# Performance work log

Measured on AMD Instinct MI355X. Metric: run time of the kernel, lower is better.

Reference implementation:

```python
import jax, jax.numpy as jnp
import numpy as np

B = 2048   # batch
C = 64     # EEG channels (num_eegch)
T = 125    # time samples -> pool5 -> 25 -> (p=5, 5)
H = 8      # num_heads
L = 6      # num_layers
D = 16     # num_projected_features
QK = 8     # qkv_len
P = 5      # tokens before cls
EPS = 1e-5


def setup_inputs() -> dict:
    key = jax.random.key(0)
    ks = iter(jax.random.split(key, 64))

    def nrm(shape, s=0.05):
        return jax.random.normal(next(ks), shape, jnp.float32) * s

    return {
        "x": jax.random.normal(next(ks), (B, 1, C, T), jnp.float32),
        "conv_t_w": nrm((8, 1, 1, 63)),
        "conv_t_b": nrm((8,)),
        "bn1_g": 1.0 + nrm((8,)),
        "bn1_b": nrm((8,)),
        "bn1_m": nrm((8,)),
        "bn1_v": 1.0 + 0.1 * jax.random.uniform(next(ks), (8,), jnp.float32),
        "conv_s_w": nrm((16, 1, C, 1)),
        "conv_s_b": nrm((16,)),
        "bn2_g": 1.0 + nrm((16,)),
        "bn2_b": nrm((16,)),
        "bn2_m": nrm((16,)),
        "bn2_v": 1.0 + 0.1 * jax.random.uniform(next(ks), (16,), jnp.float32),
        "proj_w": nrm((D, 16 * 5)),
        "proj_b": nrm((D,)),
        "cls_token": nrm((1, 1, D), 1.0),
        "pe": nrm((1, P + 1, D), 1.0),
        "qkv_w": nrm((L, 3 * H * QK, D)),
        "qkv_b": nrm((L, 3 * H * QK)),
        "out_w": nrm((L, D, H * QK)),
        "out_b": nrm((L, D)),
        "ln1_g": jnp.ones((L, D), jnp.float32),
        "ln1_b": jnp.zeros((L, D), jnp.float32),
        "ln2_g": jnp.ones((L, D), jnp.float32),
        "ln2_b": jnp.zeros((L, D), jnp.float32),
        "mlp_w1": nrm((L, 2 * D, D)),
        "mlp_b1": nrm((L, 2 * D)),
        "mlp_w2": nrm((L, D, 2 * D)),
        "mlp_b2": nrm((L, D)),
        "head_ln_g": jnp.ones((D,), jnp.float32),
        "head_ln_b": jnp.zeros((D,), jnp.float32),
        "head_w": nrm((2, D)),
        "head_b": nrm((2,)),
    }


def _bn(z, g, b, m, v):
    s = (g * jax.lax.rsqrt(v + EPS))[None, :, None, None]
    return (z - m[None, :, None, None]) * s + b[None, :, None, None]


def _ln(z, g, b):
    m = z.mean(-1, keepdims=True)
    var = jnp.mean((z - m) ** 2, -1, keepdims=True)
    return (z - m) * jax.lax.rsqrt(var + EPS) * g + b


def _forward(x, conv_t_w, conv_t_b, bn1_g, bn1_b, bn1_m, bn1_v,
             conv_s_w, conv_s_b, bn2_g, bn2_b, bn2_m, bn2_v,
             proj_w, proj_b, cls_token, pe,
             qkv_w, qkv_b, out_w, out_b, ln1_g, ln1_b, ln2_g, ln2_b,
             mlp_w1, mlp_b1, mlp_w2, mlp_b2,
             head_ln_g, head_ln_b, head_w, head_b):
    b = x.shape[0]
    dn = ('NCHW', 'OIHW', 'NCHW')
    # temporal conv, 'same' padding on width (kernel 63 -> pad 31/31)
    y = jax.lax.conv_general_dilated(x, conv_t_w, (1, 1), [(0, 0), (31, 31)], dimension_numbers=dn)
    y = _bn(y + conv_t_b[None, :, None, None], bn1_g, bn1_b, bn1_m, bn1_v)
    # grouped spatial conv collapses the EEG-channel axis
    y = jax.lax.conv_general_dilated(y, conv_s_w, (1, 1), 'VALID', dimension_numbers=dn, feature_group_count=8)
    y = _bn(y + conv_s_b[None, :, None, None], bn2_g, bn2_b, bn2_m, bn2_v)
    y = jax.nn.elu(y)                              # (b,16,1,125)
    y = y.reshape(b, 16, 1, T // 5, 5).mean(-1)    # avg_pool2d (1,5) -> (b,16,1,25)
    # dropout: identity at inference
    y = y.reshape(b, 16, 1, P, 5)
    y = jnp.swapaxes(y, 3, 4)
    tok = jnp.swapaxes(y.reshape(b, 16 * 5, P), 1, 2)   # (b,5,80)
    tok = tok @ proj_w.T + proj_b                       # (b,5,16)
    z = jnp.concatenate([jnp.broadcast_to(cls_token, (b, 1, D)), tok], axis=1) + pe  # (b,6,16)
    scale = QK ** -0.5
    for i in range(L):
        h1 = _ln(z, ln1_g[i], ln1_b[i])
        qkv = h1 @ qkv_w[i].T + qkv_b[i]                # (b,6,3*H*QK)
        q, k, v = jnp.split(qkv, 3, axis=-1)
        q = q.reshape(b, P + 1, H, QK).transpose(0, 2, 1, 3)
        k = k.reshape(b, P + 1, H, QK).transpose(0, 2, 1, 3)
        v = v.reshape(b, P + 1, H, QK).transpose(0, 2, 1, 3)
        att = jax.nn.softmax(jnp.einsum('bhsd,bhtd->bhst', q, k) * scale, axis=-1)
        o = jnp.einsum('bhst,bhtd->bhsd', att, v).transpose(0, 2, 1, 3).reshape(b, P + 1, H * QK)
        z = o @ out_w[i].T + out_b[i] + z
        h2 = _ln(z, ln2_g[i], ln2_b[i])
        m = jax.nn.gelu(h2 @ mlp_w1[i].T + mlp_b1[i], approximate=False) @ mlp_w2[i].T + mlp_b2[i]
        z = m + z
    cls = _ln(z[:, 0, :], head_ln_g, head_ln_b)
    return jax.nn.softmax(cls @ head_w.T + head_b, axis=-1)


def reference(x, conv_t_w, conv_t_b, bn1_g, bn1_b, bn1_m, bn1_v,
              conv_s_w, conv_s_b, bn2_g, bn2_b, bn2_m, bn2_v,
              proj_w, proj_b, cls_token, pe,
              qkv_w, qkv_b, out_w, out_b, ln1_g, ln1_b, ln2_g, ln2_b,
              mlp_w1, mlp_b1, mlp_w2, mlp_b2,
              head_ln_g, head_ln_b, head_w, head_b):
    return _forward(x, conv_t_w, conv_t_b, bn1_g, bn1_b, bn1_m, bn1_v,
                    conv_s_w, conv_s_b, bn2_g, bn2_b, bn2_m, bn2_v,
                    proj_w, proj_b, cls_token, pe,
                    qkv_w, qkv_b, out_w, out_b, ln1_g, ln1_b, ln2_g, ln2_b,
                    mlp_w1, mlp_b1, mlp_w2, mlp_b2,
                    head_ln_g, head_ln_b, head_w, head_b)
```

## Files before the change

### kernel.cpp

```cpp
#include <hip/hip_runtime.h>

#define WAVE_SYNC() do { asm volatile("" ::: "memory"); \
                         __builtin_amdgcn_wave_barrier(); \
                         asm volatile("" ::: "memory"); } while (0)

__device__ __forceinline__ float ln_norm16(float z, float g, float bb) {
    float s = z, q = z * z;
    #pragma unroll
    for (int off = 8; off >= 1; off >>= 1) {
        s += __shfl_xor(s, off, 16);
        q += __shfl_xor(q, off, 16);
    }
    float mean = s * 0.0625f;
    float var  = q * 0.0625f - mean * mean;
    return (z - mean) * rsqrtf(var + 1e-5f) * g + bb;
}

__device__ __forceinline__ float gelu_exact(float a) {
    float xa = fabsf(a) * 0.70710678118654752f;
    float tt = 1.f / (1.f + 0.3275911f * xa);
    float poly = tt * (0.254829592f + tt * (-0.284496736f + tt * (1.421413741f
               + tt * (-1.453152027f + tt * 1.061405429f))));
    float erfv = 1.f - poly * __expf(-xa * xa);
    erfv = a >= 0.f ? erfv : -erfv;
    return 0.5f * a * (1.f + erfv);
}

__device__ __forceinline__ float dot16(const float* h, float4 w0, float4 w1,
                                       float4 w2, float4 w3) {
    return h[0]*w0.x + h[1]*w0.y + h[2]*w0.z + h[3]*w0.w
         + h[4]*w1.x + h[5]*w1.y + h[6]*w1.z + h[7]*w1.w
         + h[8]*w2.x + h[9]*w2.y + h[10]*w2.z + h[11]*w2.w
         + h[12]*w3.x + h[13]*w3.y + h[14]*w3.z + h[15]*w3.w;
}

#define FXSP  0
#define FPOOL 3136
#define F_TOT 3584

extern "C" __global__ __launch_bounds__(128, 2)
void eegnet_frontend(
    const float* __restrict__ x,
    const float* __restrict__ conv_t_w, const float* __restrict__ conv_t_b,
    const float* __restrict__ bn1_g, const float* __restrict__ bn1_b,
    const float* __restrict__ bn1_m, const float* __restrict__ bn1_v,
    const float* __restrict__ conv_s_w, const float* __restrict__ conv_s_b,
    const float* __restrict__ bn2_g, const float* __restrict__ bn2_b,
    const float* __restrict__ bn2_m, const float* __restrict__ bn2_v,
    const float* __restrict__ proj_w, const float* __restrict__ proj_b,
    float* __restrict__ tokws)
{
    __shared__ __align__(16) float sm[F_TOT];
    const int b   = blockIdx.x;
    const int tid = threadIdx.x;

    for (int i = tid; i < 16 * 71; i += 128) {
        int row = i / 71, k = i - row * 71;
        int off = (k < 32) ? k : (k + 125);
        sm[FXSP + row * 196 + off] = 0.f;
    }

    {
        const float* xb = x + (size_t)b * 8000;
        const int t = min(tid, 124);
        float a0[16];
        #pragma unroll
        for (int o = 0; o < 16; ++o) a0[o] = 0.f;
        #pragma unroll 8
        for (int c = 0; c < 64; ++c) {
            float xv = xb[c * 125 + t];
            #pragma unroll
            for (int o = 0; o < 16; ++o)
                a0[o] += conv_s_w[o * 64 + c] * xv;
        }
        if (tid < 125) {
            #pragma unroll
            for (int o = 0; o < 16; ++o)
                sm[FXSP + o * 196 + 32 + t] = a0[o];
        }
    }

    const int oo = tid & 15, qg = tid >> 4, gg = oo >> 1;
    float sa, cc;
    {
        float s1 = bn1_g[gg] * rsqrtf(bn1_v[gg] + 1e-5f);
        float b1 = (conv_t_b[gg] - bn1_m[gg]) * s1 + bn1_b[gg];
        float s2 = bn2_g[oo] * rsqrtf(bn2_v[oo] + 1e-5f);
        float ssum = 0.f;
        const float4* csw = reinterpret_cast<const float4*>(conv_s_w + oo * 64);
        #pragma unroll
        for (int i = 0; i < 16; ++i) {
            float4 v = csw[i];
            ssum += v.x + v.y + v.z + v.w;
        }
        sa = s1 * s2;
        cc = (b1 * ssum + conv_s_b[oo] - bn2_m[oo]) * s2 + bn2_b[oo];
    }
    float wt[63];
    #pragma unroll
    for (int k = 0; k < 63; ++k) wt[k] = conv_t_w[gg * 63 + k];

    __syncthreads();

    #pragma unroll 1
    for (int jj = 0; jj < 4; ++jj) {
        int j = qg + 8 * jj;
        if (j < 25) {
            int base = FXSP + oo * 196 + 5 * j + 1;
            float acc5[5] = {0.f, 0.f, 0.f, 0.f, 0.f};
            #pragma unroll
            for (int m = 0; m < 67; ++m) {
                float xv = sm[base + m];
                #pragma unroll
                for (int uu = 0; uu < 5; ++uu)
                    if (uu <= m && m - uu <= 62) acc5[uu] += wt[m - uu] * xv;
            }
            float psum = 0.f;
            #pragma unroll
            for (int uu = 0; uu < 5; ++uu) {
                float v = acc5[uu] * sa + cc;
                psum += (v > 0.f) ? v : (__expf(v) - 1.f);
            }
            sm[FPOOL + oo * 28 + j] = psum * 0.2f;
        }
    }

    __syncthreads();

    if (tid < 80) {
        int p = tid >> 4, dd = tid & 15;
        float acc = proj_b[dd];
        const float4* wp = reinterpret_cast<const float4*>(proj_w + dd * 80);
        #pragma unroll
        for (int i = 0; i < 20; ++i) {
            float4 w4 = wp[i];
            acc += w4.x * sm[FPOOL + ((4*i+0)/5) * 28 + p * 5 + ((4*i+0)%5)];
            acc += w4.y * sm[FPOOL + ((4*i+1)/5) * 28 + p * 5 + ((4*i+1)%5)];
            acc += w4.z * sm[FPOOL + ((4*i+2)/5) * 28 + p * 5 + ((4*i+2)%5)];
            acc += w4.w * sm[FPOOL + ((4*i+3)/5) * 28 + p * 5 + ((4*i+3)%5)];
        }
        tokws[b * 80 + tid] = acc;
    }
}

#define WQKV 0
#define BQKV 3840
#define WOUT 4032
#define BOUT 5120
#define WM1  5136
#define BM1  5776
#define WM2  5808
#define BM2  6384
#define LN1G 6400
#define LN1B 6416
#define LN2G 6432
#define LN2B 6448
#define WEND 6464
#define SSTR 1568
#define SH1  0
#define SQKV 128
#define SMHS 1312
#define T_TOT (WEND + 4*SSTR)

extern "C" __global__ __launch_bounds__(256, 2)
void eegnet_transformer(
    const float* __restrict__ cls_token, const float* __restrict__ pe,
    const float* __restrict__ qkv_w, const float* __restrict__ qkv_b,
    const float* __restrict__ out_w, const float* __restrict__ out_b,
    const float* __restrict__ ln1_g, const float* __restrict__ ln1_b,
    const float* __restrict__ ln2_g, const float* __restrict__ ln2_b,
    const float* __restrict__ mlp_w1, const float* __restrict__ mlp_b1,
    const float* __restrict__ mlp_w2, const float* __restrict__ mlp_b2,
    const float* __restrict__ head_ln_g, const float* __restrict__ head_ln_b,
    const float* __restrict__ head_w, const float* __restrict__ head_b,
    const float* __restrict__ tokws, float* __restrict__ out)
{
    __shared__ __align__(16) float sm[T_TOT];
    const int tid = threadIdx.x;
    const int ss  = tid >> 7;
    const int u   = tid & 127;
    const int sA  = blockIdx.x * 4 + ss * 2;
    const int d16 = u & 15, qg = u >> 4;
    const int t6c = min(qg, 5);
    const int wav = u >> 6, al = u & 63;
    const int sbA = WEND + (ss * 2    ) * SSTR;
    const int sbB = WEND + (ss * 2 + 1) * SSTR;

    float zA, zB;
    {
        float peV = pe[t6c * 16 + d16];
        if (t6c == 0) {
            float cv = cls_token[d16];
            zA = cv + peV; zB = cv + peV;
        } else {
            zA = tokws[(sA    ) * 80 + (t6c - 1) * 16 + d16] + peV;
            zB = tokws[(sA + 1) * 80 + (t6c - 1) * 16 + d16] + peV;
        }
    }

    #pragma unroll 1
    for (int li = 0; li < 6; ++li) {
        __syncthreads();

        {
            const float4* s1 = reinterpret_cast<const float4*>(qkv_w + li * 3072);
            #pragma unroll
            for (int it = 0; it < 3; ++it) {
                int i = tid + it * 256;
                float4 v = s1[i];
                int j = i >> 2, k = (i & 3) << 2;
                *reinterpret_cast<float4*>(&sm[WQKV + j * 20 + k]) = v;
            }
            {
                float4 v = reinterpret_cast<const float4*>(out_w + li * 1024)[tid];
                int j = tid >> 4, k = (tid & 15) << 2;
                *reinterpret_cast<float4*>(&sm[WOUT + j * 68 + k]) = v;
            }
            if (tid < 128) {
                float4 v = reinterpret_cast<const float4*>(mlp_w1 + li * 512)[tid];
                int j = tid >> 2, k = (tid & 3) << 2;
                *reinterpret_cast<float4*>(&sm[WM1 + j * 20 + k]) = v;
            } else {
                int i = tid - 128;
                float4 v = reinterpret_cast<const float4*>(mlp_w2 + li * 512)[i];
                int j = i >> 3, k = (i & 7) << 2;
                *reinterpret_cast<float4*>(&sm[WM2 + j * 36 + k]) = v;
            }
            if (tid < 192) sm[BQKV + tid] = qkv_b[li * 192 + tid];
            else if (tid < 208) sm[BOUT + tid - 192] = out_b[li * 16 + tid - 192];
            else if (tid < 240) sm[BM1 + tid - 208]  = mlp_b1[li * 32 + tid - 208];
            else               sm[BM2 + tid - 240]  = mlp_b2[li * 16 + tid - 240];
            if (tid >= 64 && tid < 80)        sm[LN1G + tid - 64]  = ln1_g[li * 16 + tid - 64];
            else if (tid >= 80 && tid < 96)   sm[LN1B + tid - 80]  = ln1_b[li * 16 + tid - 80];
            else if (tid >= 96 && tid < 112)  sm[LN2G + tid - 96]  = ln2_g[li * 16 + tid - 96];
            else if (tid >= 112 && tid < 128) sm[LN2B + tid - 112] = ln2_b[li * 16 + tid - 112];
        }
        __syncthreads();

        {
            float g = sm[LN1G + d16], bb = sm[LN1B + d16];
            sm[sbA + SH1 + t6c * 20 + d16] = ln_norm16(zA, g, bb);
            sm[sbB + SH1 + t6c * 20 + d16] = ln_norm16(zB, g, bb);
        }
        WAVE_SYNC();

        float hrA[16], hrB[16];
        {
            const float4* pA = reinterpret_cast<const float4*>(&sm[sbA + SH1 + t6c * 20]);
            const float4* pB = reinterpret_cast<const float4*>(&sm[sbB + SH1 + t6c * 20]);
            #pragma unroll
            for (int i = 0; i < 4; ++i) {
                float4 va = pA[i], vb = pB[i];
                hrA[4*i+0]=va.x; hrA[4*i+1]=va.y; hrA[4*i+2]=va.z; hrA[4*i+3]=va.w;
                hrB[4*i+0]=vb.x; hrB[4*i+1]=vb.y; hrB[4*i+2]=vb.z; hrB[4*i+3]=vb.w;
            }
        }

        #pragma unroll 2
        for (int r = 0; r < 12; ++r) {
            int j = d16 + 16 * r;
            const float4* wp = reinterpret_cast<const float4*>(&sm[WQKV + j * 20]);
            float4 w0 = wp[0], w1_ = wp[1], w2_ = wp[2], w3_ = wp[3];
            float bb = sm[BQKV + j];
            sm[sbA + SQKV + t6c * 196 + j] = bb + dot16(hrA, w0, w1_, w2_, w3_);
            sm[sbB + SQKV + t6c * 196 + j] = bb + dot16(hrB, w0, w1_, w2_, w3_);
        }
        __syncthreads();

        {
            bool act = (wav == 0) ? (al < 32) : (al < 16);
            if (act) {
                int h  = al & 7;
                int qs = (wav == 0) ? (al >> 3) : 4 + (al >> 3);
                const int qoffA = sbA + SQKV + qs * 196 + h * 8;
                const int qoffB = sbB + SQKV + qs * 196 + h * 8;
                const float4* qpA = reinterpret_cast<const float4*>(&sm[qoffA]);
                const float4* qpB = reinterpret_cast<const float4*>(&sm[qoffB]);
                float4 qA0 = qpA[0], qA1 = qpA[1], qB0 = qpB[0], qB1 = qpB[1];
                float scA[6], scB[6];
                #pragma unroll
                for (int t = 0; t < 6; ++t) {
                    const float4* kA = reinterpret_cast<const float4*>(&sm[sbA + SQKV + t * 196 + 64 + h * 8]);
                    const float4* kB = reinterpret_cast<const float4*>(&sm[sbB + SQKV + t * 196 + 64 + h * 8]);
                    float4 a0 = kA[0], a1 = kA[1], b0 = kB[0], b1 = kB[1];
                    scA[t] = (qA0.x*a0.x + qA0.y*a0.y + qA0.z*a0.z + qA0.w*a0.w
                            + qA1.x*a1.x + qA1.y*a1.y + qA1.z*a1.z + qA1.w*a1.w)
                            * 0.35355339059327373f;
                    scB[t] = (qB0.x*b0.x + qB0.y*b0.y + qB0.z*b0.z + qB0.w*b0.w
                            + qB1.x*b1.x + qB1.y*b1.y + qB1.z*b1.z + qB1.w*b1.w)
                            * 0.35355339059327373f;
                }
                float mxA = scA[0], mxB = scB[0];
                #pragma unroll
                for (int t = 1; t < 6; ++t) { mxA = fmaxf(mxA, scA[t]); mxB = fmaxf(mxB, scB[t]); }
                float suA = 0.f, suB = 0.f;
                #pragma unroll
                for (int t = 0; t < 6; ++t) {
                    scA[t] = __expf(scA[t] - mxA); suA += scA[t];
                    scB[t] = __expf(scB[t] - mxB); suB += scB[t];
                }
                float ivA = 1.f / suA, ivB = 1.f / suB;
                float oA[8] = {0,0,0,0,0,0,0,0}, oB[8] = {0,0,0,0,0,0,0,0};
                #pragma unroll
                for (int t = 0; t < 6; ++t) {
                    const float4* vA = reinterpret_cast<const float4*>(&sm[sbA + SQKV + t * 196 + 128 + h * 8]);
                    const float4* vB = reinterpret_cast<const float4*>(&sm[sbB + SQKV + t * 196 + 128 + h * 8]);
                    float4 a0 = vA[0], a1 = vA[1], b0 = vB[0], b1 = vB[1];
                    float aa = scA[t] * ivA, ab = scB[t] * ivB;
                    oA[0]+=aa*a0.x; oA[1]+=aa*a0.y; oA[2]+=aa*a0.z; oA[3]+=aa*a0.w;
                    oA[4]+=aa*a1.x; oA[5]+=aa*a1.y; oA[6]+=aa*a1.z; oA[7]+=aa*a1.w;
                    oB[0]+=ab*b0.x; oB[1]+=ab*b0.y; oB[2]+=ab*b0.z; oB[3]+=ab*b0.w;
                    oB[4]+=ab*b1.x; oB[5]+=ab*b1.y; oB[6]+=ab*b1.z; oB[7]+=ab*b1.w;
                }
                *reinterpret_cast<float4*>(&sm[qoffA    ]) = float4{oA[0],oA[1],oA[2],oA[3]};
                *reinterpret_cast<float4*>(&sm[qoffA + 4]) = float4{oA[4],oA[5],oA[6],oA[7]};
                *reinterpret_cast<float4*>(&sm[qoffB    ]) = float4{oB[0],oB[1],oB[2],oB[3]};
                *reinterpret_cast<float4*>(&sm[qoffB + 4]) = float4{oB[4],oB[5],oB[6],oB[7]};
            }
        }
        WAVE_SYNC();

        {
            const float4* wop = reinterpret_cast<const float4*>(&sm[WOUT + d16 * 68]);
            const float4* oaA = reinterpret_cast<const float4*>(&sm[sbA + SQKV + t6c * 196]);
            const float4* oaB = reinterpret_cast<const float4*>(&sm[sbB + SQKV + t6c * 196]);
            float bb = sm[BOUT + d16];
            float aA = bb, aB = bb;
            #pragma unroll 4
            for (int i = 0; i < 16; ++i) {
                float4 w = wop[i];
                float4 va = oaA[i], vb = oaB[i];
                aA += va.x*w.x + va.y*w.y + va.z*w.z + va.w*w.w;
                aB += vb.x*w.x + vb.y*w.y + vb.z*w.z + vb.w*w.w;
            }
            zA += aA; zB += aB;
        }

        {
            float g = sm[LN2G + d16], bb = sm[LN2B + d16];
            sm[sbA + SH1 + t6c * 20 + d16] = ln_norm16(zA, g, bb);
            sm[sbB + SH1 + t6c * 20 + d16] = ln_norm16(zB, g, bb);
        }
        WAVE_SYNC();
        {
            const float4* pA = reinterpret_cast<const float4*>(&sm[sbA + SH1 + t6c * 20]);
            const float4* pB = reinterpret_cast<const float4*>(&sm[sbB + SH1 + t6c * 20]);
            #pragma unroll
            for (int i = 0; i < 4; ++i) {
                float4 va = pA[i], vb = pB[i];
                hrA[4*i+0]=va.x; hrA[4*i+1]=va.y; hrA[4*i+2]=va.z; hrA[4*i+3]=va.w;
                hrB[4*i+0]=vb.x; hrB[4*i+1]=vb.y; hrB[4*i+2]=vb.z; hrB[4*i+3]=vb.w;
            }
        }

        #pragma unroll
        for (int r = 0; r < 2; ++r) {
            int uu = d16 + 16 * r;
            const float4* wp = reinterpret_cast<const float4*>(&sm[WM1 + uu * 20]);
            float4 w0 = wp[0], w1_ = wp[1], w2_ = wp[2], w3_ = wp[3];
            float bb = sm[BM1 + uu];
            float aA = bb + dot16(hrA, w0, w1_, w2_, w3_);
            float aB = bb + dot16(hrB, w0, w1_, w2_, w3_);
            sm[sbA + SMHS + t6c * 36 + uu] = gelu_exact(aA);
            sm[sbB + SMHS + t6c * 36 + uu] = gelu_exact(aB);
        }
        WAVE_SYNC();

        {
            const float4* wp = reinterpret_cast<const float4*>(&sm[WM2 + d16 * 36]);
            const float4* mA = reinterpret_cast<const float4*>(&sm[sbA + SMHS + t6c * 36]);
            const float4* mB = reinterpret_cast<const float4*>(&sm[sbB + SMHS + t6c * 36]);
            float bb = sm[BM2 + d16];
            float aA = bb, aB = bb;
            #pragma unroll
            for (int i = 0; i < 8; ++i) {
                float4 w = wp[i];
                float4 va = mA[i], vb = mB[i];
                aA += va.x*w.x + va.y*w.y + va.z*w.z + va.w*w.w;
                aB += vb.x*w.x + vb.y*w.y + vb.z*w.z + vb.w*w.w;
            }
            zA += aA; zB += aB;
        }
    }

    if (u < 16) {
        float g = head_ln_g[d16], bb = head_ln_b[d16];
        float w0 = head_w[d16], w1 = head_w[16 + d16];
        float cvA = ln_norm16(zA, g, bb);
        float cvB = ln_norm16(zB, g, bb);
        float pA0 = cvA * w0, pA1 = cvA * w1;
        float pB0 = cvB * w0, pB1 = cvB * w1;
        #pragma unroll
        for (int off = 8; off >= 1; off >>= 1) {
            pA0 += __shfl_xor(pA0, off, 16);
            pA1 += __shfl_xor(pA1, off, 16);
            pB0 += __shfl_xor(pB0, off, 16);
            pB1 += __shfl_xor(pB1, off, 16);
        }
        if (u == 0) {
            float hb0 = head_b[0], hb1 = head_b[1];
            {
                float l0 = pA0 + hb0, l1 = pA1 + hb1;
                float mx = fmaxf(l0, l1);
                float e0 = __expf(l0 - mx), e1 = __expf(l1 - mx);
                float inv = 1.f / (e0 + e1);
                out[sA * 2 + 0] = e0 * inv;
                out[sA * 2 + 1] = e1 * inv;
            }
            {
                float l0 = pB0 + hb0, l1 = pB1 + hb1;
                float mx = fmaxf(l0, l1);
                float e0 = __expf(l0 - mx), e1 = __expf(l1 - mx);
                float inv = 1.f / (e0 + e1);
                out[(sA + 1) * 2 + 0] = e0 * inv;
                out[(sA + 1) * 2 + 1] = e1 * inv;
            }
        }
    }
}

extern "C" void kernel_launch(void* const* d_in, const int* in_sizes, int n_in,
                              void* d_out, int out_size, void* d_ws, size_t ws_size,
                              hipStream_t stream) {
    (void)n_in; (void)ws_size; (void)out_size;
    const float* a0  = (const float*)d_in[0];
    const float* a1  = (const float*)d_in[1];
    const float* a2  = (const float*)d_in[2];
    const float* a3  = (const float*)d_in[3];
    const float* a4  = (const float*)d_in[4];
    const float* a5  = (const float*)d_in[5];
    const float* a6  = (const float*)d_in[6];
    const float* a7  = (const float*)d_in[7];
    const float* a8  = (const float*)d_in[8];
    const float* a9  = (const float*)d_in[9];
    const float* a10 = (const float*)d_in[10];
    const float* a11 = (const float*)d_in[11];
    const float* a12 = (const float*)d_in[12];
    const float* a13 = (const float*)d_in[13];
    const float* a14 = (const float*)d_in[14];
    const float* a15 = (const float*)d_in[15];
    const float* a16 = (const float*)d_in[16];
    const float* a17 = (const float*)d_in[17];
    const float* a18 = (const float*)d_in[18];
    const float* a19 = (const float*)d_in[19];
    const float* a20 = (const float*)d_in[20];
    const float* a21 = (const float*)d_in[21];
    const float* a22 = (const float*)d_in[22];
    const float* a23 = (const float*)d_in[23];
    const float* a24 = (const float*)d_in[24];
    const float* a25 = (const float*)d_in[25];
    const float* a26 = (const float*)d_in[26];
    const float* a27 = (const float*)d_in[27];
    const float* a28 = (const float*)d_in[28];
    const float* a29 = (const float*)d_in[29];
    const float* a30 = (const float*)d_in[30];
    const float* a31 = (const float*)d_in[31];
    const float* a32 = (const float*)d_in[32];

    int Bn = in_sizes[0] / (64 * 125);
    float* tokws = (float*)d_ws;

    eegnet_frontend<<<Bn, 128, 0, stream>>>(
        a0, a1, a2, a3, a4, a5, a6, a7, a8, a9, a10, a11, a12, a13, a14, tokws);

    eegnet_transformer<<<Bn / 4, 256, 0, stream>>>(
        a15, a16, a17, a18, a19, a20, a21, a22, a23, a24, a25, a26, a27, a28,
        a29, a30, a31, a32, tokws, (float*)d_out);
}
```

Measured before the change: 242.9 us.

## Run frontend with one 64-lane wavefront per sample and wave-level sync

The frontend kernel now runs one 64-thread wavefront per batch sample instead of 128 threads. Each lane computes two time columns of the spatial conv, seven pooled outputs of the temporal conv, and two projection outputs. Block-wide __syncthreads is replaced by a wave barrier, which removes cross-wave synchronisation and halves the thread count per sample. The trade-off is more serial work per lane, some redundant clamped iterations, and lower parallelism per block on a kernel that may already be latency-bound.

```diff
diff --git a/kernel.cpp b/kernel.cpp
--- a/kernel.cpp
+++ b/kernel.cpp
@@ -34,11 +34,11 @@
          + h[12]*w3.x + h[13]*w3.y + h[14]*w3.z + h[15]*w3.w;
 }
 
-#define FXSP  0
-#define FPOOL 3136
-#define F_TOT 3584
-
-extern "C" __global__ __launch_bounds__(128, 2)
+#define F_XS  0
+#define F_PL  3168
+#define F_TOT 3616
+
+extern "C" __global__ __launch_bounds__(64, 2)
 void eegnet_frontend(
     const float* __restrict__ x,
     const float* __restrict__ conv_t_w, const float* __restrict__ conv_t_b,
@@ -51,36 +51,40 @@
     float* __restrict__ tokws)
 {
     __shared__ __align__(16) float sm[F_TOT];
-    const int b   = blockIdx.x;
-    const int tid = threadIdx.x;
-
-    for (int i = tid; i < 16 * 71; i += 128) {
-        int row = i / 71, k = i - row * 71;
+    const int b    = blockIdx.x;
+    const int lane = threadIdx.x;
+
+    for (int i = lane; i < 16 * 73; i += 64) {
+        int row = i / 73, k = i - row * 73;
         int off = (k < 32) ? k : (k + 125);
-        sm[FXSP + row * 196 + off] = 0.f;
+        sm[F_XS + row * 198 + off] = 0.f;
     }
 
     {
         const float* xb = x + (size_t)b * 8000;
-        const int t = min(tid, 124);
-        float a0[16];
-        #pragma unroll
-        for (int o = 0; o < 16; ++o) a0[o] = 0.f;
-        #pragma unroll 8
+        const int l2 = min(lane, 60);
+        float a0[16], a1[16];
+        #pragma unroll
+        for (int o = 0; o < 16; ++o) { a0[o] = 0.f; a1[o] = 0.f; }
+        #pragma unroll 16
         for (int c = 0; c < 64; ++c) {
-            float xv = xb[c * 125 + t];
-            #pragma unroll
-            for (int o = 0; o < 16; ++o)
-                a0[o] += conv_s_w[o * 64 + c] * xv;
-        }
-        if (tid < 125) {
-            #pragma unroll
-            for (int o = 0; o < 16; ++o)
-                sm[FXSP + o * 196 + 32 + t] = a0[o];
-        }
-    }
-
-    const int oo = tid & 15, qg = tid >> 4, gg = oo >> 1;
+            float xv0 = xb[c * 125 + lane];
+            float xv1 = xb[c * 125 + 64 + l2];
+            #pragma unroll
+            for (int o = 0; o < 16; ++o) {
+                float w = conv_s_w[o * 64 + c];
+                a0[o] += w * xv0;
+                a1[o] += w * xv1;
+            }
+        }
+        #pragma unroll
+        for (int o = 0; o < 16; ++o) {
+            sm[F_XS + o * 198 + 32 + lane] = a0[o];
+            if (lane < 61) sm[F_XS + o * 198 + 96 + lane] = a1[o];
+        }
+    }
+
+    const int oo = lane & 15, qg = lane >> 4, gg = oo >> 1;
     float sa, cc;
     {
         float s1 = bn1_g[gg] * rsqrtf(bn1_v[gg] + 1e-5f);
@@ -100,46 +104,49 @@
     #pragma unroll
     for (int k = 0; k < 63; ++k) wt[k] = conv_t_w[gg * 63 + k];
 
-    __syncthreads();
+    WAVE_SYNC();
 
     #pragma unroll 1
-    for (int jj = 0; jj < 4; ++jj) {
-        int j = qg + 8 * jj;
-        if (j < 25) {
-            int base = FXSP + oo * 196 + 5 * j + 1;
-            float acc5[5] = {0.f, 0.f, 0.f, 0.f, 0.f};
-            #pragma unroll
-            for (int m = 0; m < 67; ++m) {
-                float xv = sm[base + m];
-                #pragma unroll
-                for (int uu = 0; uu < 5; ++uu)
-                    if (uu <= m && m - uu <= 62) acc5[uu] += wt[m - uu] * xv;
-            }
-            float psum = 0.f;
-            #pragma unroll
-            for (int uu = 0; uu < 5; ++uu) {
-                float v = acc5[uu] * sa + cc;
-                psum += (v > 0.f) ? v : (__expf(v) - 1.f);
-            }
-            sm[FPOOL + oo * 28 + j] = psum * 0.2f;
-        }
-    }
-
-    __syncthreads();
-
-    if (tid < 80) {
-        int p = tid >> 4, dd = tid & 15;
+    for (int jj = 0; jj < 7; ++jj) {
+        int j  = qg * 7 + jj;
+        int jc = min(j, 24);
+        int base = F_XS + oo * 198 + 5 * jc + 1;
+        float acc5[5] = {0.f, 0.f, 0.f, 0.f, 0.f};
+        #pragma unroll
+        for (int m = 0; m < 67; ++m) {
+            float xv = sm[base + m];
+            #pragma unroll
+            for (int u = 0; u < 5; ++u)
+                if (u <= m && m - u <= 62) acc5[u] += wt[m - u] * xv;
+        }
+        float psum = 0.f;
+        #pragma unroll
+        for (int u = 0; u < 5; ++u) {
+            float v = acc5[u] * sa + cc;
+            psum += (v > 0.f) ? v : (__expf(v) - 1.f);
+        }
+        if (j == jc) sm[F_PL + oo * 28 + j] = psum * 0.2f;
+    }
+
+    WAVE_SYNC();
+
+    #pragma unroll
+    for (int pass = 0; pass < 2; ++pass) {
+        int oi = (pass == 0) ? lane : (64 + lane);
+        int p = oi >> 4, dd = oi & 15;
+        int pc = min(p, 4);
+        bool act = (pass == 0) || (lane < 16);
         float acc = proj_b[dd];
         const float4* wp = reinterpret_cast<const float4*>(proj_w + dd * 80);
         #pragma unroll
         for (int i = 0; i < 20; ++i) {
             float4 w4 = wp[i];
-            acc += w4.x * sm[FPOOL + ((4*i+0)/5) * 28 + p * 5 + ((4*i+0)%5)];
-            acc += w4.y * sm[FPOOL + ((4*i+1)/5) * 28 + p * 5 + ((4*i+1)%5)];
-            acc += w4.z * sm[FPOOL + ((4*i+2)/5) * 28 + p * 5 + ((4*i+2)%5)];
-            acc += w4.w * sm[FPOOL + ((4*i+3)/5) * 28 + p * 5 + ((4*i+3)%5)];
-        }
-        tokws[b * 80 + tid] = acc;
+            acc += w4.x * sm[F_PL + ((4*i+0)/5) * 28 + pc * 5 + ((4*i+0)%5)];
+            acc += w4.y * sm[F_PL + ((4*i+1)/5) * 28 + pc * 5 + ((4*i+1)%5)];
+            acc += w4.z * sm[F_PL + ((4*i+2)/5) * 28 + pc * 5 + ((4*i+2)%5)];
+            acc += w4.w * sm[F_PL + ((4*i+3)/5) * 28 + pc * 5 + ((4*i+3)%5)];
+        }
+        if (act) tokws[b * 80 + pc * 16 + dd] = acc;
     }
 }
 
@@ -460,7 +467,7 @@
     int Bn = in_sizes[0] / (64 * 125);
     float* tokws = (float*)d_ws;
 
-    eegnet_frontend<<<Bn, 128, 0, stream>>>(
+    eegnet_frontend<<<Bn, 64, 0, stream>>>(
         a0, a1, a2, a3, a4, a5, a6, a7, a8, a9, a10, a11, a12, a13, a14, tokws);
 
     eegnet_transformer<<<Bn / 4, 256, 0, stream>>>(
```

Result: faster. 233.0 us (-4.1%).
